# Kernel optimization log

Measured on AMD Instinct MI355X. Metric: run time of the kernel, lower is better.

Reference implementation:

```python
import jax, jax.numpy as jnp
import numpy as np

VTH = 1.0  # config['v_threshold']
DT = 1.0


def spike_fn(x):
    # forward of ActFun_adp: heaviside(mem - vth)
    return (x > 0).astype(x.dtype)


def setup_inputs() -> dict:
    key = jax.random.key(0)
    k0, k1, k2, k3, k4 = jax.random.split(key, 5)
    B, T, D, H, O = 256, 250, 700, 1024, 20
    input_data = jax.random.normal(k0, (B, T, D), dtype=jnp.float32)
    # dense_1: nn.Linear(700, hidden) default init ~ U(-1/sqrt(D), 1/sqrt(D)); normal/sqrt(D) is an equivalent-scale stand-in
    W1 = jax.random.normal(k1, (H, D), dtype=jnp.float32) / np.sqrt(D).astype(np.float32)
    b1 = jnp.zeros((H,), dtype=jnp.float32)
    tau_m1 = jax.random.uniform(k2, (H,), dtype=jnp.float32, minval=0.0, maxval=4.0)
    # dense_2: xavier_normal_ weight, zero bias
    W2 = jax.random.normal(k3, (O, H), dtype=jnp.float32) * np.sqrt(2.0 / (H + O)).astype(np.float32)
    b2 = jnp.zeros((O,), dtype=jnp.float32)
    tau_m2 = jax.random.uniform(k4, (O,), dtype=jnp.float32, minval=0.0, maxval=4.0)
    return {"input_data": input_data, "W1": W1, "b1": b1, "tau_m1": tau_m1,
            "W2": W2, "b2": b2, "tau_m2": tau_m2}


def reference(input_data, W1, b1, tau_m1, W2, b2, tau_m2):
    B, T, D = input_data.shape
    H = W1.shape[0]
    O = W2.shape[0]
    alpha1 = jax.nn.sigmoid(tau_m1)  # [H]
    alpha2 = jax.nn.sigmoid(tau_m2)  # [O]
    # dense_1 is time-invariant: precompute projections for all timesteps [T,B,H]
    d1_all = (jnp.einsum('btd,hd->bth', input_data, W1) + b1).transpose(1, 0, 2)

    def step(carry, xs):
        mem1, spk1, mem2, acc = carry
        d1_t, i = xs
        # LIF layer 1: soft reset via -vth*spike (mem_update_pra, R_m=1, dt=1)
        mem1 = mem1 * alpha1 + (1.0 - alpha1) * d1_t - VTH * spk1 * DT
        spk1 = spike_fn(mem1 - VTH)
        # readout integrator
        d2 = spk1 @ W2.T + b2
        mem2 = mem2 * alpha2 + (1.0 - alpha2) * d2
        # accumulate softmax for i > 10
        gate = jnp.where(i > 10, jnp.float32(1.0), jnp.float32(0.0))
        acc = acc + gate * jax.nn.softmax(mem2, axis=1)
        return (mem1, spk1, mem2, acc), None

    init = (jnp.zeros((B, H), jnp.float32), jnp.zeros((B, H), jnp.float32),
            jnp.zeros((B, O), jnp.float32), jnp.zeros((B, O), jnp.float32))
    (_, _, _, acc), _ = jax.lax.scan(step, init, (d1_all, jnp.arange(T)))
    return acc
```

## Files before the change

kernel.cpp:

```cpp
#include <hip/hip_runtime.h>
#include <hip/hip_bf16.h>

#define B_  256
#define T_  250
#define D_  700
#define H_  1024
#define O_  20
#define KP  704
#define M_  64000

typedef __attribute__((ext_vector_type(8))) short bf16x8;
typedef __attribute__((ext_vector_type(4))) float f32x4;

__device__ __forceinline__ void gl_lds16(const void* g, void* l) {
    __builtin_amdgcn_global_load_lds(
        (const __attribute__((address_space(1))) unsigned int*)g,
        (__attribute__((address_space(3))) unsigned int*)l, 16, 0, 0);
}

__global__ void split_convert(const float* __restrict__ src,
                              unsigned short* __restrict__ hi,
                              unsigned short* __restrict__ lo,
                              int M, int Kin, int Kout)
{
    int idx = blockIdx.x * blockDim.x + threadIdx.x;
    int chunks = Kout >> 3;
    int total = M * chunks;
    if (idx >= total) return;
    int m  = idx / chunks;
    int c  = idx - m * chunks;
    int d0 = c << 3;
    float x[8];
    if (d0 + 8 <= Kin) {
        const float4* p = (const float4*)(src + (long)m * Kin + d0);
        float4 v0 = p[0], v1 = p[1];
        x[0] = v0.x; x[1] = v0.y; x[2] = v0.z; x[3] = v0.w;
        x[4] = v1.x; x[5] = v1.y; x[6] = v1.z; x[7] = v1.w;
    } else {
#pragma unroll
        for (int e = 0; e < 8; ++e) {
            int d = d0 + e;
            x[e] = (d < Kin) ? src[(long)m * Kin + d] : 0.0f;
        }
    }
    unsigned short h8[8], l8[8];
#pragma unroll
    for (int e = 0; e < 8; ++e) {
        __hip_bfloat16 h = __float2bfloat16(x[e]);
        float hf = __bfloat162float(h);
        __hip_bfloat16 lv = __float2bfloat16(x[e] - hf);
        h8[e] = *(unsigned short*)&h;
        l8[e] = *(unsigned short*)&lv;
    }
    long ob = (long)m * Kout + d0;
    *(uint4*)(hi + ob) = *(uint4*)h8;
    *(uint4*)(lo + ob) = *(uint4*)l8;
}

__global__ __launch_bounds__(256, 2) void gemm_split(
    const unsigned short* __restrict__ Ahi, const unsigned short* __restrict__ Alo,
    const unsigned short* __restrict__ Bhi, const unsigned short* __restrict__ Blo,
    const float* __restrict__ bias, float* __restrict__ C)
{
    __shared__ __align__(16) unsigned short sAh[128 * 32];
    __shared__ __align__(16) unsigned short sAl[128 * 32];
    __shared__ __align__(16) unsigned short sBh[128 * 32];
    __shared__ __align__(16) unsigned short sBl[128 * 32];

    const int t    = threadIdx.x;
    const int nblk = blockIdx.x;
    const int mblk = blockIdx.y;
    const int wave = t >> 6, lane = t & 63;
    const int wr = wave >> 1, wc = wave & 1;

    f32x4 acc[4][4];
#pragma unroll
    for (int i = 0; i < 4; ++i)
#pragma unroll
        for (int j = 0; j < 4; ++j) acc[i][j] = (f32x4){0.f, 0.f, 0.f, 0.f};

    const long arow = (long)(mblk * 128 + (t >> 2)) * KP + (t & 3) * 8;
    const long brow = (long)(nblk * 128 + (t >> 2)) * KP + (t & 3) * 8;
    const int  l8   = t * 8;

    const int fr = lane & 15;
    const int fk = (lane >> 4) * 8;

    for (int ks = 0; ks < KP; ks += 32) {
        __syncthreads();
        gl_lds16(Ahi + arow + ks, &sAh[l8]);
        gl_lds16(Ahi + arow + 64 * KP + ks, &sAh[2048 + l8]);
        gl_lds16(Alo + arow + ks, &sAl[l8]);
        gl_lds16(Alo + arow + 64 * KP + ks, &sAl[2048 + l8]);
        gl_lds16(Bhi + brow + ks, &sBh[l8]);
        gl_lds16(Bhi + brow + 64 * KP + ks, &sBh[2048 + l8]);
        gl_lds16(Blo + brow + ks, &sBl[l8]);
        gl_lds16(Blo + brow + 64 * KP + ks, &sBl[2048 + l8]);
        __syncthreads();

        bf16x8 ah[4], al[4], bh[4], bl[4];
#pragma unroll
        for (int i = 0; i < 4; ++i) {
            ah[i] = *(const bf16x8*)&sAh[(wr * 64 + i * 16 + fr) * 32 + fk];
            al[i] = *(const bf16x8*)&sAl[(wr * 64 + i * 16 + fr) * 32 + fk];
            bh[i] = *(const bf16x8*)&sBh[(wc * 64 + i * 16 + fr) * 32 + fk];
            bl[i] = *(const bf16x8*)&sBl[(wc * 64 + i * 16 + fr) * 32 + fk];
        }
#pragma unroll
        for (int i = 0; i < 4; ++i)
#pragma unroll
            for (int j = 0; j < 4; ++j)
                acc[i][j] = __builtin_amdgcn_mfma_f32_16x16x32_bf16(ah[i], bh[j], acc[i][j], 0, 0, 0);
#pragma unroll
        for (int i = 0; i < 4; ++i)
#pragma unroll
            for (int j = 0; j < 4; ++j)
                acc[i][j] = __builtin_amdgcn_mfma_f32_16x16x32_bf16(ah[i], bl[j], acc[i][j], 0, 0, 0);
#pragma unroll
        for (int i = 0; i < 4; ++i)
#pragma unroll
            for (int j = 0; j < 4; ++j)
                acc[i][j] = __builtin_amdgcn_mfma_f32_16x16x32_bf16(al[i], bh[j], acc[i][j], 0, 0, 0);
    }

    const int r0 = mblk * 128 + wr * 64 + (lane >> 4) * 4;
    const int c0 = nblk * 128 + wc * 64 + (lane & 15);
#pragma unroll
    for (int j = 0; j < 4; ++j) {
        int col = c0 + j * 16;
        float bv = bias[col];
#pragma unroll
        for (int i = 0; i < 4; ++i) {
            int row = r0 + i * 16;
#pragma unroll
            for (int r = 0; r < 4; ++r)
                C[(long)(row + r) * H_ + col] = acc[i][j][r] + bv;
        }
    }
}

__global__ __launch_bounds__(256) void lif_spikes(
    const float* __restrict__ d1,
    const float* __restrict__ tau1,
    unsigned long long* __restrict__ spk)
{
    const int b    = blockIdx.y;
    const int h    = blockIdx.x * 256 + threadIdx.x;
    const int lane = threadIdx.x & 63;
    const int widx = blockIdx.x * 4 + (threadIdx.x >> 6);

    float tv  = tau1[h];
    float a1  = 1.0f / (1.0f + __expf(-tv));
    float om1 = 1.0f - a1;
    float mem = 0.f, sp = 0.f;

    const float* dp = d1 + (long)b * T_ * H_ + h;
    unsigned long long* op = spk + (long)b * T_ * 16 + widx;

    float p0 = dp[0], p1 = dp[1L * H_], p2 = dp[2L * H_], p3 = dp[3L * H_];

    for (int ts = 0; ts < T_; ++ts) {
        float cur = p0; p0 = p1; p1 = p2; p2 = p3;
        int nts = ts + 4; nts = (nts < T_) ? nts : (T_ - 1);
        p3 = dp[(long)nts * H_];

        mem = mem * a1 + om1 * cur - sp;
        sp  = (mem > 1.0f) ? 1.0f : 0.0f;
        unsigned long long msk = __ballot(mem > 1.0f);
        if (lane == 0) op[(long)ts * 16] = msk;
    }
}

__global__ __launch_bounds__(256) void readout_dots(
    const unsigned long long* __restrict__ spk,
    const float* __restrict__ W2,
    float* __restrict__ d2t)
{
    const int t = threadIdx.x, wave = t >> 6, lane = t & 63;

    float w2r[5][16];
#pragma unroll
    for (int oo = 0; oo < 5; ++oo)
#pragma unroll
        for (int q = 0; q < 4; ++q)
            *(float4*)&w2r[oo][4 * q] =
                *(const float4*)&W2[(wave * 5 + oo) * H_ + lane * 16 + 4 * q];

    const int rbase = blockIdx.x * 64;
    for (int i = 0; i < 64; ++i) {
        int r = rbase + i;
        unsigned long long bw = spk[(long)r * 16 + (lane >> 2)];
        unsigned int bits = (unsigned int)(bw >> ((lane & 3) * 16)) & 0xFFFFu;
        float pa[5] = {0.f, 0.f, 0.f, 0.f, 0.f};
#pragma unroll
        for (int j = 0; j < 16; ++j) {
            float f = (bits >> j) & 1u ? 1.0f : 0.0f;
#pragma unroll
            for (int oo = 0; oo < 5; ++oo)
                pa[oo] = fmaf(f, w2r[oo][j], pa[oo]);
        }
#pragma unroll
        for (int m = 1; m < 64; m <<= 1)
#pragma unroll
            for (int oo = 0; oo < 5; ++oo)
                pa[oo] += __shfl_xor(pa[oo], m, 64);
        if (lane == 0) {
            int b  = r / T_;
            int ts = r - b * T_;
#pragma unroll
            for (int oo = 0; oo < 5; ++oo)
                d2t[(long)(wave * 5 + oo) * M_ + ts * 256 + b] = pa[oo];
        }
    }
}

__global__ __launch_bounds__(256) void mem2_scan(
    const float* __restrict__ d2t,
    const float* __restrict__ tau2, const float* __restrict__ b2,
    float* __restrict__ m2t)
{
    const int o = blockIdx.x;
    const int b = threadIdx.x;
    float tv  = tau2[o];
    float a2  = 1.0f / (1.0f + __expf(-tv));
    float om2 = 1.0f - a2;
    float bv  = b2[o];

    const float* dp = d2t + (long)o * M_ + b;
    float*       mp = m2t + (long)o * M_ + b;
    float mem = 0.f;

    float p0 = dp[0], p1 = dp[256], p2 = dp[512], p3 = dp[768];
    for (int ts = 0; ts < T_; ++ts) {
        float cur = p0; p0 = p1; p1 = p2; p2 = p3;
        int nts = ts + 4; nts = (nts < T_) ? nts : (T_ - 1);
        p3 = dp[(long)nts * 256];
        mem = mem * a2 + om2 * (cur + bv);
        mp[(long)ts * 256] = mem;
    }
}

__global__ __launch_bounds__(256) void softmax_acc(
    const float* __restrict__ m2t,
    float* __restrict__ out)
{
    __shared__ float sp[T_][O_];
    const int b  = blockIdx.x;
    const int ts = threadIdx.x;

    if (ts < T_) {
        if (ts > 10) {
            float m[O_];
#pragma unroll
            for (int o = 0; o < O_; ++o)
                m[o] = m2t[(long)o * M_ + ts * 256 + b];
            float mx = m[0];
#pragma unroll
            for (int o = 1; o < O_; ++o) mx = fmaxf(mx, m[o]);
            float s = 0.f;
#pragma unroll
            for (int o = 0; o < O_; ++o) { m[o] = __expf(m[o] - mx); s += m[o]; }
            float inv = 1.0f / s;
#pragma unroll
            for (int o = 0; o < O_; ++o) sp[ts][o] = m[o] * inv;
        } else {
#pragma unroll
            for (int o = 0; o < O_; ++o) sp[ts][o] = 0.f;
        }
    }
    __syncthreads();
    if (ts < O_) {
        float s = 0.f;
        for (int k = 11; k < T_; ++k) s += sp[k][ts];
        out[b * O_ + ts] = s;
    }
}

extern "C" void kernel_launch(void* const* d_in, const int* in_sizes, int n_in,
                              void* d_out, int out_size, void* d_ws, size_t ws_size,
                              hipStream_t stream)
{
    const float* X    = (const float*)d_in[0];
    const float* W1   = (const float*)d_in[1];
    const float* b1   = (const float*)d_in[2];
    const float* tau1 = (const float*)d_in[3];
    const float* W2   = (const float*)d_in[4];
    const float* b2   = (const float*)d_in[5];
    const float* tau2 = (const float*)d_in[6];
    float* out = (float*)d_out;

    unsigned short* Xhi  = (unsigned short*)d_ws;
    unsigned short* Xlo  = Xhi + (long)M_ * KP;
    unsigned short* W1hi = Xlo + (long)M_ * KP;
    unsigned short* W1lo = W1hi + (long)H_ * KP;
    float* d1 = (float*)(W1lo + (long)H_ * KP);

    unsigned long long* spk = (unsigned long long*)Xhi;
    float* d2t = (float*)Xlo;
    float* m2t = d2t + (long)O_ * M_;

    {
        int chunks = M_ * (KP / 8);
        split_convert<<<(chunks + 255) / 256, 256, 0, stream>>>(X, Xhi, Xlo, M_, D_, KP);
    }
    {
        int chunks = H_ * (KP / 8);
        split_convert<<<(chunks + 255) / 256, 256, 0, stream>>>(W1, W1hi, W1lo, H_, D_, KP);
    }

    {
        dim3 grid(H_ / 128, M_ / 128);
        gemm_split<<<grid, 256, 0, stream>>>(Xhi, Xlo, W1hi, W1lo, b1, d1);
    }

    {
        dim3 grid(H_ / 256, B_);
        lif_spikes<<<grid, 256, 0, stream>>>(d1, tau1, spk);
    }

    readout_dots<<<M_ / 64, 256, 0, stream>>>(spk, W2, d2t);

    mem2_scan<<<O_, 256, 0, stream>>>(d2t, tau2, b2, m2t);

    softmax_acc<<<B_, 256, 0, stream>>>(m2t, out);
}
```

Measured before the change: 807.3 us.

## Tune occupancy, prefetch depth and parallel split across GEMM, LIF, readout and scan kernels

The split-bf16 GEMM now requests 4 waves per SIMD and loads A fragments per row-tile instead of all at once, reducing live registers. The LIF kernel prefetches six timesteps ahead instead of four to hide more global latency. The readout kernel processes two rows per iteration with half as many rows per block, doubling the grid. The mem2 scan is split into 64-thread blocks over a 2D grid for more concurrent CUs. Higher occupancy targets may force spills in the GEMM, and the readout index arithmetic assumes at most one batch boundary crossing per pair.

After: 798.2 us. No clear change (-1.1%).

```diff
diff --git a/kernel.cpp b/kernel.cpp
--- a/kernel.cpp
+++ b/kernel.cpp
@@ -57,7 +57,7 @@
     *(uint4*)(lo + ob) = *(uint4*)l8;
 }
 
-__global__ __launch_bounds__(256, 2) void gemm_split(
+__global__ __launch_bounds__(256, 4) void gemm_split(
     const unsigned short* __restrict__ Ahi, const unsigned short* __restrict__ Alo,
     const unsigned short* __restrict__ Bhi, const unsigned short* __restrict__ Blo,
     const float* __restrict__ bias, float* __restrict__ C)
@@ -98,29 +98,26 @@
         gl_lds16(Blo + brow + 64 * KP + ks, &sBl[2048 + l8]);
         __syncthreads();
 
-        bf16x8 ah[4], al[4], bh[4], bl[4];
+        bf16x8 bh[4], bl[4];
+#pragma unroll
+        for (int j = 0; j < 4; ++j) {
+            bh[j] = *(const bf16x8*)&sBh[(wc * 64 + j * 16 + fr) * 32 + fk];
+            bl[j] = *(const bf16x8*)&sBl[(wc * 64 + j * 16 + fr) * 32 + fk];
+        }
 #pragma unroll
         for (int i = 0; i < 4; ++i) {
-            ah[i] = *(const bf16x8*)&sAh[(wr * 64 + i * 16 + fr) * 32 + fk];
-            al[i] = *(const bf16x8*)&sAl[(wr * 64 + i * 16 + fr) * 32 + fk];
-            bh[i] = *(const bf16x8*)&sBh[(wc * 64 + i * 16 + fr) * 32 + fk];
-            bl[i] = *(const bf16x8*)&sBl[(wc * 64 + i * 16 + fr) * 32 + fk];
-        }
-#pragma unroll
-        for (int i = 0; i < 4; ++i)
+            bf16x8 ah = *(const bf16x8*)&sAh[(wr * 64 + i * 16 + fr) * 32 + fk];
+            bf16x8 al = *(const bf16x8*)&sAl[(wr * 64 + i * 16 + fr) * 32 + fk];
 #pragma unroll
             for (int j = 0; j < 4; ++j)
-                acc[i][j] = __builtin_amdgcn_mfma_f32_16x16x32_bf16(ah[i], bh[j], acc[i][j], 0, 0, 0);
-#pragma unroll
-        for (int i = 0; i < 4; ++i)
+                acc[i][j] = __builtin_amdgcn_mfma_f32_16x16x32_bf16(ah, bh[j], acc[i][j], 0, 0, 0);
 #pragma unroll
             for (int j = 0; j < 4; ++j)
-                acc[i][j] = __builtin_amdgcn_mfma_f32_16x16x32_bf16(ah[i], bl[j], acc[i][j], 0, 0, 0);
-#pragma unroll
-        for (int i = 0; i < 4; ++i)
+                acc[i][j] = __builtin_amdgcn_mfma_f32_16x16x32_bf16(ah, bl[j], acc[i][j], 0, 0, 0);
 #pragma unroll
             for (int j = 0; j < 4; ++j)
-                acc[i][j] = __builtin_amdgcn_mfma_f32_16x16x32_bf16(al[i], bh[j], acc[i][j], 0, 0, 0);
+                acc[i][j] = __builtin_amdgcn_mfma_f32_16x16x32_bf16(al, bh[j], acc[i][j], 0, 0, 0);
+        }
     }
 
     const int r0 = mblk * 128 + wr * 64 + (lane >> 4) * 4;
@@ -157,12 +154,14 @@
     const float* dp = d1 + (long)b * T_ * H_ + h;
     unsigned long long* op = spk + (long)b * T_ * 16 + widx;
 
-    float p0 = dp[0], p1 = dp[1L * H_], p2 = dp[2L * H_], p3 = dp[3L * H_];
+    float p0 = dp[0],        p1 = dp[1L * H_], p2 = dp[2L * H_];
+    float p3 = dp[3L * H_],  p4 = dp[4L * H_], p5 = dp[5L * H_];
 
     for (int ts = 0; ts < T_; ++ts) {
-        float cur = p0; p0 = p1; p1 = p2; p2 = p3;
-        int nts = ts + 4; nts = (nts < T_) ? nts : (T_ - 1);
-        p3 = dp[(long)nts * H_];
+        float cur = p0;
+        p0 = p1; p1 = p2; p2 = p3; p3 = p4; p4 = p5;
+        int nts = ts + 6; nts = (nts < T_) ? nts : (T_ - 1);
+        p5 = dp[(long)nts * H_];
 
         mem = mem * a1 + om1 * cur - sp;
         sp  = (mem > 1.0f) ? 1.0f : 0.0f;
@@ -186,41 +185,55 @@
             *(float4*)&w2r[oo][4 * q] =
                 *(const float4*)&W2[(wave * 5 + oo) * H_ + lane * 16 + 4 * q];
 
-    const int rbase = blockIdx.x * 64;
-    for (int i = 0; i < 64; ++i) {
-        int r = rbase + i;
-        unsigned long long bw = spk[(long)r * 16 + (lane >> 2)];
-        unsigned int bits = (unsigned int)(bw >> ((lane & 3) * 16)) & 0xFFFFu;
-        float pa[5] = {0.f, 0.f, 0.f, 0.f, 0.f};
+    const int rbase = blockIdx.x * 32;
+    int b0 = rbase / T_;
+    int ts0 = rbase - b0 * T_;
+
+    for (int i = 0; i < 32; i += 2) {
+        int r0 = rbase + i, r1 = r0 + 1;
+        unsigned long long bw0 = spk[(long)r0 * 16 + (lane >> 2)];
+        unsigned long long bw1 = spk[(long)r1 * 16 + (lane >> 2)];
+        unsigned int bits0 = (unsigned int)(bw0 >> ((lane & 3) * 16)) & 0xFFFFu;
+        unsigned int bits1 = (unsigned int)(bw1 >> ((lane & 3) * 16)) & 0xFFFFu;
+        float pa0[5] = {0, 0, 0, 0, 0}, pa1[5] = {0, 0, 0, 0, 0};
 #pragma unroll
         for (int j = 0; j < 16; ++j) {
-            float f = (bits >> j) & 1u ? 1.0f : 0.0f;
-#pragma unroll
-            for (int oo = 0; oo < 5; ++oo)
-                pa[oo] = fmaf(f, w2r[oo][j], pa[oo]);
+            float f0 = (bits0 >> j) & 1u ? 1.0f : 0.0f;
+            float f1 = (bits1 >> j) & 1u ? 1.0f : 0.0f;
+#pragma unroll
+            for (int oo = 0; oo < 5; ++oo) {
+                pa0[oo] = fmaf(f0, w2r[oo][j], pa0[oo]);
+                pa1[oo] = fmaf(f1, w2r[oo][j], pa1[oo]);
+            }
         }
 #pragma unroll
         for (int m = 1; m < 64; m <<= 1)
 #pragma unroll
-            for (int oo = 0; oo < 5; ++oo)
-                pa[oo] += __shfl_xor(pa[oo], m, 64);
+            for (int oo = 0; oo < 5; ++oo) {
+                pa0[oo] += __shfl_xor(pa0[oo], m, 64);
+                pa1[oo] += __shfl_xor(pa1[oo], m, 64);
+            }
         if (lane == 0) {
-            int b  = r / T_;
-            int ts = r - b * T_;
-#pragma unroll
-            for (int oo = 0; oo < 5; ++oo)
-                d2t[(long)(wave * 5 + oo) * M_ + ts * 256 + b] = pa[oo];
-        }
-    }
-}
-
-__global__ __launch_bounds__(256) void mem2_scan(
+            int bA = b0, tsA = ts0 + i;
+            if (tsA >= T_) { tsA -= T_; bA += 1; }
+            int bB = bA, tsB = tsA + 1;
+            if (tsB >= T_) { tsB = 0; bB += 1; }
+#pragma unroll
+            for (int oo = 0; oo < 5; ++oo) {
+                d2t[(long)(wave * 5 + oo) * M_ + tsA * 256 + bA] = pa0[oo];
+                d2t[(long)(wave * 5 + oo) * M_ + tsB * 256 + bB] = pa1[oo];
+            }
+        }
+    }
+}
+
+__global__ __launch_bounds__(64) void mem2_scan(
     const float* __restrict__ d2t,
     const float* __restrict__ tau2, const float* __restrict__ b2,
     float* __restrict__ m2t)
 {
     const int o = blockIdx.x;
-    const int b = threadIdx.x;
+    const int b = blockIdx.y * 64 + threadIdx.x;
     float tv  = tau2[o];
     float a2  = 1.0f / (1.0f + __expf(-tv));
     float om2 = 1.0f - a2;
@@ -318,9 +331,12 @@
         lif_spikes<<<grid, 256, 0, stream>>>(d1, tau1, spk);
     }
 
-    readout_dots<<<M_ / 64, 256, 0, stream>>>(spk, W2, d2t);
-
-    mem2_scan<<<O_, 256, 0, stream>>>(d2t, tau2, b2, m2t);
+    readout_dots<<<M_ / 32, 256, 0, stream>>>(spk, W2, d2t);
+
+    {
+        dim3 grid(O_, 4);
+        mem2_scan<<<grid, 64, 0, stream>>>(d2t, tau2, b2, m2t);
+    }
 
     softmax_acc<<<B_, 256, 0, stream>>>(m2t, out);
 }
```
